# Kernel tuning notes

Hardware: AMD Instinct MI355X
Metric: run time of the kernel (lower is better)

## Reference

```python
import jax, jax.numpy as jnp
import numpy as np

NEG_INF = float(np.finfo(np.float32).min)


def setup_inputs() -> dict:
    key = jax.random.key(0)
    k1, k2, k3 = jax.random.split(key, 3)
    n_context, d_model = 4096, 2048
    x = jax.random.normal(k1, (n_context, d_model), dtype=jnp.float32)
    # nn.Linear default init scale ~ 1/sqrt(fan_in); use small weights for numeric sanity
    W_qk = jax.random.normal(k2, (d_model, d_model), dtype=jnp.float32) / np.sqrt(d_model)
    W_ov = jax.random.normal(k3, (d_model, d_model), dtype=jnp.float32) / np.sqrt(d_model)
    return {"x": x, "W_qk": W_qk, "W_ov": W_ov}


def reference(x, W_qk, W_ov):
    # Faithful to: softmax(X @ W_qk.T @ X.T + causal_mask) @ X @ W_ov.T
    # (biases of the torch Linears are never used in forward)
    n = x.shape[0]
    q = x @ W_qk.T                      # [n, d]
    scores = q @ x.T                    # [n, n]  (no 1/sqrt(d) scaling, as in source)
    causal = jnp.tril(jnp.ones((n, n), dtype=bool))
    scores = jnp.where(causal, scores, NEG_INF)  # additive -inf mask equivalent
    attn = jax.nn.softmax(scores, axis=-1)       # [n, n]
    out = (attn @ x) @ W_ov.T                    # [n, d]
    return out
```

## Files before the change

### kernel.cpp

```cpp
#include <hip/hip_runtime.h>
#include <hip/hip_bf16.h>
#include <stdint.h>
#include <stddef.h>

typedef _Float16 f16;
typedef __attribute__((ext_vector_type(8))) _Float16 f16x8;
typedef __attribute__((ext_vector_type(4))) float    f32x4;

constexpr int BM = 128, BN = 128, BK = 64;

#define GLOAD_LDS16(gp, lp)                                        \
    __builtin_amdgcn_global_load_lds(                              \
        (const __attribute__((address_space(1))) unsigned int*)(gp),\
        (__attribute__((address_space(3))) unsigned int*)(lp), 16, 0, 0)

#define MFMA_TILE(AV, BV)                                                     \
    do {                                                                      \
        __builtin_amdgcn_s_setprio(1);                                        \
        _Pragma("unroll")                                                     \
        for (int mi_ = 0; mi_ < 4; ++mi_)                                     \
            _Pragma("unroll")                                                 \
            for (int ni_ = 0; ni_ < 4; ++ni_)                                 \
                acc[mi_][ni_] = __builtin_amdgcn_mfma_f32_16x16x32_f16(       \
                    (AV)[mi_], (BV)[ni_], acc[mi_][ni_], 0, 0, 0);            \
        __builtin_amdgcn_s_setprio(0);                                        \
    } while (0)

template <int EPI, bool CAUSAL>
__global__ __launch_bounds__(512, 2) void gemm8_a2(
    const f16* __restrict__ Ah, const f16* __restrict__ Al,
    const f16* __restrict__ B,
    float* __restrict__ Cf, f16* __restrict__ Co, f16* __restrict__ Clo,
    int M, int N, int K)
{
    const int bx = blockIdx.x;
    const int by = blockIdx.y;
    if (CAUSAL && 2 * bx > by) return;

    const int tid   = threadIdx.x;
    const int lane  = tid & 63;
    const int wave  = tid >> 6;
    const int wm    = wave >> 2;
    const int wn    = wave & 3;
    const int lrow  = lane & 15;
    const int lquad = lane >> 4;

    __shared__ f16 lds[2][32768];

    const int row0 = by * 128;
    const int col0 = bx * 256;

    const int srow = tid >> 3;
    const int scol = ((tid & 7) ^ (srow & 7)) * 8;
    const int loff = wave * 512;

    const int g0 = ((lquad)     ^ (lrow & 7)) * 8;
    const int g1 = ((4 + lquad) ^ (lrow & 7)) * 8;

    const int arow = (wm * 64 + lrow) * 64;
    const int brow = (wn * 64 + lrow) * 64 + 16384;

    const f16* gAh = Ah + (size_t)(row0 + srow) * K + scol;
    const f16* gAl = Al + (size_t)(row0 + srow) * K + scol;
    const f16* gB  = B  + (size_t)(col0 + srow) * K + scol;
    const size_t r64 = (size_t)64 * K;

    f32x4 acc[4][4];
    const f32x4 fz = {0.f, 0.f, 0.f, 0.f};
    #pragma unroll
    for (int i = 0; i < 4; ++i)
        #pragma unroll
        for (int j = 0; j < 4; ++j) acc[i][j] = fz;

    const int nt = K / 64;

    #pragma unroll
    for (int u = 0; u < 4; ++u)
        GLOAD_LDS16(gB + u * r64, &lds[0][16384 + u * 4096 + loff]);
    #pragma unroll
    for (int u = 0; u < 2; ++u)
        GLOAD_LDS16(gAh + u * r64, &lds[0][u * 4096 + loff]);
    #pragma unroll
    for (int u = 0; u < 2; ++u)
        GLOAD_LDS16(gAl + u * r64, &lds[0][8192 + u * 4096 + loff]);
    asm volatile("s_waitcnt vmcnt(2)");
    __builtin_amdgcn_s_barrier();

    auto tile_body = [&](int t, bool stage) {
        const int cur = t & 1;
        const size_t kn = (size_t)(t + 1) * 64;
        const f16* bufc = &lds[cur][0];
        f16* bufn = &lds[cur ^ 1][0];

        f16x8 av[4], bv0[4], bv1[4];

        #pragma unroll
        for (int mi = 0; mi < 4; ++mi)
            av[mi] = *(const f16x8*)&bufc[arow + mi * 1024 + g0];
        #pragma unroll
        for (int ni = 0; ni < 4; ++ni)
            bv0[ni] = *(const f16x8*)&bufc[brow + ni * 1024 + g0];
        if (stage) {
            GLOAD_LDS16(gB + kn,       &bufn[16384 + loff]);
            GLOAD_LDS16(gB + r64 + kn, &bufn[16384 + 4096 + loff]);
        }
        __builtin_amdgcn_s_barrier();
        asm volatile("s_waitcnt lgkmcnt(0)");
        MFMA_TILE(av, bv0);
        __builtin_amdgcn_s_barrier();

        #pragma unroll
        for (int mi = 0; mi < 4; ++mi)
            av[mi] = *(const f16x8*)&bufc[arow + mi * 1024 + g1];
        #pragma unroll
        for (int ni = 0; ni < 4; ++ni)
            bv1[ni] = *(const f16x8*)&bufc[brow + ni * 1024 + g1];
        if (stage) {
            GLOAD_LDS16(gB + 2 * r64 + kn, &bufn[16384 +  8192 + loff]);
            GLOAD_LDS16(gB + 3 * r64 + kn, &bufn[16384 + 12288 + loff]);
            asm volatile("s_waitcnt vmcnt(4)");
        } else {
            asm volatile("s_waitcnt vmcnt(0)");
        }
        __builtin_amdgcn_s_barrier();
        asm volatile("s_waitcnt lgkmcnt(0)");
        MFMA_TILE(av, bv1);
        __builtin_amdgcn_s_barrier();

        #pragma unroll
        for (int mi = 0; mi < 4; ++mi)
            av[mi] = *(const f16x8*)&bufc[8192 + arow + mi * 1024 + g0];
        if (stage) {
            GLOAD_LDS16(gAh + kn,       &bufn[loff]);
            GLOAD_LDS16(gAh + r64 + kn, &bufn[4096 + loff]);
        }
        __builtin_amdgcn_s_barrier();
        asm volatile("s_waitcnt lgkmcnt(0)");
        MFMA_TILE(av, bv0);
        __builtin_amdgcn_s_barrier();

        #pragma unroll
        for (int mi = 0; mi < 4; ++mi)
            av[mi] = *(const f16x8*)&bufc[8192 + arow + mi * 1024 + g1];
        if (stage) {
            GLOAD_LDS16(gAl + kn,       &bufn[ 8192 + loff]);
            GLOAD_LDS16(gAl + r64 + kn, &bufn[12288 + loff]);
        }
        asm volatile("s_waitcnt vmcnt(2)");
        __builtin_amdgcn_s_barrier();
        asm volatile("s_waitcnt lgkmcnt(0)");
        MFMA_TILE(av, bv1);
        __builtin_amdgcn_s_barrier();
    };

    for (int t = 0; t < nt - 1; ++t) tile_body(t, true);
    tile_body(nt - 1, false);

    #pragma unroll
    for (int mi = 0; mi < 4; ++mi) {
        #pragma unroll
        for (int ni = 0; ni < 4; ++ni) {
            #pragma unroll
            for (int r = 0; r < 4; ++r) {
                const int row = row0 + wm * 64 + mi * 16 + lquad * 4 + r;
                const int col = col0 + wn * 64 + ni * 16 + lrow;
                const size_t idx = (size_t)row * N + col;
                const float v = acc[mi][ni][r];
                if (EPI == 0) {
                    Cf[idx] = v;
                } else {
                    const f16 h = (f16)v;
                    Co[idx]  = h;
                    Clo[idx] = (f16)(v - (float)h);
                }
            }
        }
    }
}

template <int EPI>
__global__ __launch_bounds__(512, 2) void gemm8_1t(
    const f16* __restrict__ A, const f16* __restrict__ B,
    float* __restrict__ Cf, f16* __restrict__ Co,
    int M, int N, int K)
{
    const int bx = blockIdx.x;
    const int by = blockIdx.y;

    const int tid   = threadIdx.x;
    const int lane  = tid & 63;
    const int wave  = tid >> 6;
    const int wm    = wave >> 2;
    const int wn    = wave & 3;
    const int lrow  = lane & 15;
    const int lquad = lane >> 4;

    __shared__ f16 lds[3][24576];

    const int row0 = by * 128;
    const int col0 = bx * 256;

    const int srow = tid >> 3;
    const int scol = ((tid & 7) ^ (srow & 7)) * 8;
    const int loff = wave * 512;
    const int g0 = ((lquad)     ^ (lrow & 7)) * 8;
    const int g1 = ((4 + lquad) ^ (lrow & 7)) * 8;
    const int arow = (wm * 64 + lrow) * 64;
    const int brow = (wn * 64 + lrow) * 64 + 8192;

    const f16* gA = A + (size_t)(row0 + srow) * K + scol;
    const f16* gB = B + (size_t)(col0 + srow) * K + scol;
    const size_t r64 = (size_t)64 * K;

    f32x4 acc[4][4];
    const f32x4 fz = {0.f, 0.f, 0.f, 0.f};
    #pragma unroll
    for (int i = 0; i < 4; ++i)
        #pragma unroll
        for (int j = 0; j < 4; ++j) acc[i][j] = fz;

    const int nt = K / 64;

    #pragma unroll
    for (int tt = 0; tt < 2; ++tt) {
        const size_t kk = (size_t)tt * 64;
        #pragma unroll
        for (int u = 0; u < 4; ++u)
            GLOAD_LDS16(gB + u * r64 + kk, &lds[tt][8192 + u * 4096 + loff]);
        #pragma unroll
        for (int u = 0; u < 2; ++u)
            GLOAD_LDS16(gA + u * r64 + kk, &lds[tt][u * 4096 + loff]);
    }
    asm volatile("s_waitcnt vmcnt(6)");
    __builtin_amdgcn_s_barrier();

    int cur = 0;
    for (int t = 0; t < nt; ++t) {
        const int nb = (cur >= 1) ? (cur - 1) : (cur + 2);
        const bool stage2 = (t + 2 < nt);
        const size_t kn = (size_t)(t + 2) * 64;
        const f16* bufc = &lds[cur][0];
        f16* bufn = &lds[nb][0];

        f16x8 av[4], bv[4];

        #pragma unroll
        for (int mi = 0; mi < 4; ++mi)
            av[mi] = *(const f16x8*)&bufc[arow + mi * 1024 + g0];
        #pragma unroll
        for (int ni = 0; ni < 4; ++ni)
            bv[ni] = *(const f16x8*)&bufc[brow + ni * 1024 + g0];
        if (stage2) {
            GLOAD_LDS16(gB + kn,           &bufn[8192 + loff]);
            GLOAD_LDS16(gB + r64 + kn,     &bufn[8192 + 4096 + loff]);
            GLOAD_LDS16(gB + 2 * r64 + kn, &bufn[8192 + 8192 + loff]);
        }
        __builtin_amdgcn_s_barrier();
        asm volatile("s_waitcnt lgkmcnt(0)");
        MFMA_TILE(av, bv);
        __builtin_amdgcn_s_barrier();

        #pragma unroll
        for (int mi = 0; mi < 4; ++mi)
            av[mi] = *(const f16x8*)&bufc[arow + mi * 1024 + g1];
        #pragma unroll
        for (int ni = 0; ni < 4; ++ni)
            bv[ni] = *(const f16x8*)&bufc[brow + ni * 1024 + g1];
        if (stage2) {
            GLOAD_LDS16(gB + 3 * r64 + kn, &bufn[8192 + 12288 + loff]);
            GLOAD_LDS16(gA + kn,           &bufn[loff]);
            GLOAD_LDS16(gA + r64 + kn,     &bufn[4096 + loff]);
            asm volatile("s_waitcnt vmcnt(6)");
        } else {
            asm volatile("s_waitcnt vmcnt(0)");
        }
        __builtin_amdgcn_s_barrier();
        asm volatile("s_waitcnt lgkmcnt(0)");
        MFMA_TILE(av, bv);
        __builtin_amdgcn_s_barrier();

        cur = (cur == 2) ? 0 : cur + 1;
    }

    #pragma unroll
    for (int mi = 0; mi < 4; ++mi) {
        #pragma unroll
        for (int ni = 0; ni < 4; ++ni) {
            #pragma unroll
            for (int r = 0; r < 4; ++r) {
                const int row = row0 + wm * 64 + mi * 16 + lquad * 4 + r;
                const int col = col0 + wn * 64 + ni * 16 + lrow;
                const size_t idx = (size_t)row * N + col;
                const float v = acc[mi][ni][r];
                if (EPI == 0) Cf[idx] = v;
                else          Co[idx] = (f16)v;
            }
        }
    }
}

template <int EPI, bool KCAUSAL>
__global__ __launch_bounds__(256) void gemm_plain(
    const f16* __restrict__ A, const f16* __restrict__ B,
    float* __restrict__ Cf, f16* __restrict__ Co,
    int M, int N, int K)
{
    const int bx = blockIdx.x;
    const int by = KCAUSAL ? (gridDim.y - 1 - blockIdx.y) : blockIdx.y;

    const int tid   = threadIdx.x;
    const int lane  = tid & 63;
    const int wave  = tid >> 6;
    const int wm    = wave >> 1;
    const int wn    = wave & 1;
    const int lrow  = lane & 15;
    const int lquad = lane >> 4;

    __shared__ f16 sA[BM * BK];
    __shared__ f16 sB[BN * BK];

    const int row0 = by * BM;
    const int col0 = bx * BN;

    const int srow = tid >> 3;
    const int scol = (((tid & 7) ^ ((tid >> 3) & 7))) * 8;
    const int lbase = wave * 512;

    f32x4 acc[4][4];
    const f32x4 fzero = {0.f, 0.f, 0.f, 0.f};
    #pragma unroll
    for (int i = 0; i < 4; ++i)
        #pragma unroll
        for (int j = 0; j < 4; ++j) acc[i][j] = fzero;

    const int Keff = KCAUSAL ? (by + 1) * BM : K;

    for (int k0 = 0; k0 < Keff; k0 += BK) {
        __syncthreads();
        #pragma unroll
        for (int r = 0; r < 4; ++r) {
            const int trow = srow + 32 * r;
            GLOAD_LDS16(&A[(size_t)(row0 + trow) * K + k0 + scol], &sA[lbase + r * 2048]);
            GLOAD_LDS16(&B[(size_t)(col0 + trow) * K + k0 + scol], &sB[lbase + r * 2048]);
        }
        __syncthreads();

        #pragma unroll
        for (int kk = 0; kk < 2; ++kk) {
            const int grpA = ((kk * 4 + lquad) ^ (lrow & 7)) * 8;
            f16x8 av[4], bv[4];
            #pragma unroll
            for (int mi = 0; mi < 4; ++mi)
                av[mi] = *reinterpret_cast<const f16x8*>(
                    &sA[(wm * 64 + mi * 16 + lrow) * BK + grpA]);
            #pragma unroll
            for (int ni = 0; ni < 4; ++ni)
                bv[ni] = *reinterpret_cast<const f16x8*>(
                    &sB[(wn * 64 + ni * 16 + lrow) * BK + grpA]);

            #pragma unroll
            for (int mi = 0; mi < 4; ++mi)
                #pragma unroll
                for (int ni = 0; ni < 4; ++ni)
                    acc[mi][ni] = __builtin_amdgcn_mfma_f32_16x16x32_f16(
                        av[mi], bv[ni], acc[mi][ni], 0, 0, 0);
        }
    }

    #pragma unroll
    for (int mi = 0; mi < 4; ++mi) {
        #pragma unroll
        for (int ni = 0; ni < 4; ++ni) {
            #pragma unroll
            for (int r = 0; r < 4; ++r) {
                const int row = row0 + wm * 64 + mi * 16 + lquad * 4 + r;
                const int col = col0 + wn * 64 + ni * 16 + lrow;
                const size_t idx = (size_t)row * N + col;
                const float v = acc[mi][ni][r];
                if (EPI == 0) Cf[idx] = v;
                else          Co[idx] = (f16)v;
            }
        }
    }
}

__global__ __launch_bounds__(256) void split_f32_f16(
    const float* __restrict__ in, f16* __restrict__ hi, f16* __restrict__ lo,
    size_t nelem)
{
    const size_t i = ((size_t)blockIdx.x * 256 + threadIdx.x) * 4;
    if (i >= nelem) return;
    const float4 v = *reinterpret_cast<const float4*>(in + i);
    union { f16 h[4]; ushort4 u; } H, L;
    H.h[0] = (f16)v.x; H.h[1] = (f16)v.y; H.h[2] = (f16)v.z; H.h[3] = (f16)v.w;
    *reinterpret_cast<ushort4*>(hi + i) = H.u;
    if (lo) {
        L.h[0] = (f16)(v.x - (float)H.h[0]);
        L.h[1] = (f16)(v.y - (float)H.h[1]);
        L.h[2] = (f16)(v.z - (float)H.h[2]);
        L.h[3] = (f16)(v.w - (float)H.h[3]);
        *reinterpret_cast<ushort4*>(lo + i) = L.u;
    }
}

__global__ __launch_bounds__(256) void softmax_rows(
    const float* __restrict__ S, f16* __restrict__ P, int n)
{
    const int row = blockIdx.x;
    const int len = row + 1;
    const int padlen = ((row >> 7) + 1) << 7;
    const float* srow = S + (size_t)row * n;
    f16* prow = P + (size_t)row * n;
    const int tid = threadIdx.x;
    const int lane = tid & 63, wave = tid >> 6;
    __shared__ float redm[4], reds[4];

    float m = -3.0e38f, s = 0.f;
    for (int j = tid; j < len; j += 256) {
        const float v = srow[j];
        const float mn = fmaxf(m, v);
        s = s * __expf(m - mn) + __expf(v - mn);
        m = mn;
    }
    #pragma unroll
    for (int off = 32; off; off >>= 1) {
        const float mo = __shfl_xor(m, off, 64);
        const float so = __shfl_xor(s, off, 64);
        const float mn = fmaxf(m, mo);
        s = s * __expf(m - mn) + so * __expf(mo - mn);
        m = mn;
    }
    if (lane == 0) { redm[wave] = m; reds[wave] = s; }
    __syncthreads();
    float M = redm[0], Sm = reds[0];
    #pragma unroll
    for (int w = 1; w < 4; ++w) {
        const float mn = fmaxf(M, redm[w]);
        Sm = Sm * __expf(M - mn) + reds[w] * __expf(redm[w] - mn);
        M = mn;
    }
    const float inv = 1.0f / Sm;

    const f16 z = (f16)0.0f;
    for (int j = tid; j < padlen; j += 256)
        prow[j] = (j < len) ? (f16)(__expf(srow[j] - M) * inv) : z;
}

__global__ __launch_bounds__(256) void transpose_f32_f16(
    const float* __restrict__ in, f16* __restrict__ out, int rows, int cols)
{
    __shared__ float tile[32][33];
    const int bx = blockIdx.x;
    const int by = blockIdx.y;
    const int tx = threadIdx.x & 31;
    const int ty = threadIdx.x >> 5;
    #pragma unroll
    for (int r = 0; r < 4; ++r)
        tile[ty + 8 * r][tx] = in[(size_t)(by * 32 + ty + 8 * r) * cols + bx * 32 + tx];
    __syncthreads();
    #pragma unroll
    for (int r = 0; r < 4; ++r)
        out[(size_t)(bx * 32 + ty + 8 * r) * rows + by * 32 + tx] =
            (f16)tile[tx][ty + 8 * r];
}

extern "C" void kernel_launch(void* const* d_in, const int* in_sizes, int n_in,
                              void* d_out, int out_size, void* d_ws, size_t ws_size,
                              hipStream_t stream)
{
    const int n = 4096, d = 2048;
    const float* x   = (const float*)d_in[0];
    const float* Wqk = (const float*)d_in[1];
    const float* Wov = (const float*)d_in[2];
    float* out = (float*)d_out;

    char* ws = (char*)d_ws;
    const size_t MB = 1 << 20;
    f16*   xh   = (f16*)  (ws);
    f16*   xl   = (f16*)  (ws + 16 * MB);
    f16*   Wh   = (f16*)  (ws + 32 * MB);
    f16*   Wovh = (f16*)  (ws + 40 * MB);
    f16*   xTh  = (f16*)  (ws + 48 * MB);
    f16*   qh   = (f16*)  (ws + 64 * MB);
    f16*   ql   = (f16*)  (ws + 80 * MB);
    float* S    = (float*)(ws + 96 * MB);
    f16*   P    = (f16*)  (ws);
    f16*   o    = (f16*)  (ws + 64 * MB);

    const dim3 blk(256);
    const dim3 blk8(512);

    split_f32_f16<<<dim3((n * d) / (256 * 4)), blk, 0, stream>>>(x,   xh, xl, (size_t)n * d);
    split_f32_f16<<<dim3((d * d) / (256 * 4)), blk, 0, stream>>>(Wqk, Wh, nullptr, (size_t)d * d);
    split_f32_f16<<<dim3((d * d) / (256 * 4)), blk, 0, stream>>>(Wov, Wovh, nullptr, (size_t)d * d);
    transpose_f32_f16<<<dim3(d / 32, n / 32), blk, 0, stream>>>(x, xTh, n, d);

    gemm8_a2<1, false><<<dim3(d / 256, n / 128), blk8, 0, stream>>>(
        xh, xl, Wh, nullptr, qh, ql, n, d, d);

    gemm8_a2<0, true><<<dim3(n / 256, n / 128), blk8, 0, stream>>>(
        qh, ql, xh, S, nullptr, nullptr, n, n, d);

    softmax_rows<<<dim3(n), blk, 0, stream>>>(S, P, n);

    gemm_plain<2, true><<<dim3(d / BN, n / BM), blk, 0, stream>>>(
        P, xTh, nullptr, o, n, d, n);

    gemm8_1t<0><<<dim3(d / 256, n / 128), blk8, 0, stream>>>(
        o, Wovh, out, nullptr, n, d, d);
}
```

Baseline: 420.1 us.

## Add BK=32 scores GEMM with higher occupancy and per-wave causal skip; cache softmax row

Adds a new gemm32_a2 kernel for the causal scores GEMM. It uses a K-step of 32 and half the LDS, and raises launch_bounds to 4 blocks per CU. Waves whose column slice lies entirely above the diagonal skip the LDS reads, MFMAs and stores. The softmax kernel now caches the row in LDS so global memory is read once instead of twice. The trade-offs are twice as many barrier-synchronised iterations, a full vmcnt(0) wait each step, and 16KB of extra LDS in the softmax kernel, which may lower its occupancy.

```diff
diff --git a/kernel.cpp b/kernel.cpp
--- a/kernel.cpp
+++ b/kernel.cpp
@@ -27,7 +27,7 @@
     } while (0)
 
 template <int EPI, bool CAUSAL>
-__global__ __launch_bounds__(512, 2) void gemm8_a2(
+__global__ __launch_bounds__(512, 4) void gemm32_a2(
     const f16* __restrict__ Ah, const f16* __restrict__ Al,
     const f16* __restrict__ B,
     float* __restrict__ Cf, f16* __restrict__ Co, f16* __restrict__ Clo,
@@ -45,25 +45,27 @@
     const int lrow  = lane & 15;
     const int lquad = lane >> 4;
 
-    __shared__ f16 lds[2][32768];
+    __shared__ f16 lds[2][16384];
 
     const int row0 = by * 128;
     const int col0 = bx * 256;
 
-    const int srow = tid >> 3;
-    const int scol = ((tid & 7) ^ (srow & 7)) * 8;
-    const int loff = wave * 512;
-
-    const int g0 = ((lquad)     ^ (lrow & 7)) * 8;
-    const int g1 = ((4 + lquad) ^ (lrow & 7)) * 8;
-
-    const int arow = (wm * 64 + lrow) * 64;
-    const int brow = (wn * 64 + lrow) * 64 + 16384;
-
-    const f16* gAh = Ah + (size_t)(row0 + srow) * K + scol;
-    const f16* gAl = Al + (size_t)(row0 + srow) * K + scol;
-    const f16* gB  = B  + (size_t)(col0 + srow) * K + scol;
-    const size_t r64 = (size_t)64 * K;
+    const bool liveN = !CAUSAL || (col0 + wn * 64 <= row0 + 127);
+
+    const int srA  = tid >> 3;
+    const int gl   = (tid & 7) ^ (srA & 7);
+    const int term = gl >> 2;
+    const int cg   = gl & 3;
+    const f16* pA = (term ? Al : Ah) + (size_t)(row0 + srA) * K + cg * 8;
+    const f16* pB = B + (size_t)(col0 + 2 * srA + term) * K + cg * 8;
+    const size_t uA = (size_t)64 * K;
+    const size_t uB = (size_t)128 * K;
+    const int ld0 = wave * 512;
+
+    const int aoff0 = (wm * 64 + lrow) * 64 + ((lquad ^ (lrow & 7)) * 8);
+    const int aoff1 = (wm * 64 + lrow) * 64 + (((4 + lquad) ^ (lrow & 7)) * 8);
+    const int boff  = 8192 + (wn * 32 + (lrow >> 1)) * 64 +
+                      ((((lrow & 1) * 4 + lquad) ^ ((lrow >> 1) & 7)) * 8);
 
     f32x4 acc[4][4];
     const f32x4 fz = {0.f, 0.f, 0.f, 0.f};
@@ -72,89 +74,55 @@
         #pragma unroll
         for (int j = 0; j < 4; ++j) acc[i][j] = fz;
 
-    const int nt = K / 64;
-
-    #pragma unroll
-    for (int u = 0; u < 4; ++u)
-        GLOAD_LDS16(gB + u * r64, &lds[0][16384 + u * 4096 + loff]);
-    #pragma unroll
-    for (int u = 0; u < 2; ++u)
-        GLOAD_LDS16(gAh + u * r64, &lds[0][u * 4096 + loff]);
-    #pragma unroll
-    for (int u = 0; u < 2; ++u)
-        GLOAD_LDS16(gAl + u * r64, &lds[0][8192 + u * 4096 + loff]);
-    asm volatile("s_waitcnt vmcnt(2)");
+    const int nt = K / 32;
+
+    GLOAD_LDS16(pA,      &lds[0][ld0]);
+    GLOAD_LDS16(pA + uA, &lds[0][4096 + ld0]);
+    GLOAD_LDS16(pB,      &lds[0][8192 + ld0]);
+    GLOAD_LDS16(pB + uB, &lds[0][12288 + ld0]);
+    asm volatile("s_waitcnt vmcnt(0)");
     __builtin_amdgcn_s_barrier();
 
-    auto tile_body = [&](int t, bool stage) {
-        const int cur = t & 1;
-        const size_t kn = (size_t)(t + 1) * 64;
-        const f16* bufc = &lds[cur][0];
-        f16* bufn = &lds[cur ^ 1][0];
-
-        f16x8 av[4], bv0[4], bv1[4];
-
-        #pragma unroll
-        for (int mi = 0; mi < 4; ++mi)
-            av[mi] = *(const f16x8*)&bufc[arow + mi * 1024 + g0];
-        #pragma unroll
-        for (int ni = 0; ni < 4; ++ni)
-            bv0[ni] = *(const f16x8*)&bufc[brow + ni * 1024 + g0];
+    for (int t = 0; t < nt; ++t) {
+        const f16* bufc = &lds[t & 1][0];
+        f16* bufn = &lds[(t + 1) & 1][0];
+        const bool stage = (t + 1 < nt);
+        const size_t kn = (size_t)(t + 1) * 32;
+
+        f16x8 ah[4], al[4], bv[4];
+
+        if (liveN) {
+            #pragma unroll
+            for (int mi = 0; mi < 4; ++mi)
+                ah[mi] = *(const f16x8*)&bufc[aoff0 + mi * 1024];
+            #pragma unroll
+            for (int ni = 0; ni < 4; ++ni)
+                bv[ni] = *(const f16x8*)&bufc[boff + ni * 512];
+        }
         if (stage) {
-            GLOAD_LDS16(gB + kn,       &bufn[16384 + loff]);
-            GLOAD_LDS16(gB + r64 + kn, &bufn[16384 + 4096 + loff]);
-        }
-        __builtin_amdgcn_s_barrier();
-        asm volatile("s_waitcnt lgkmcnt(0)");
-        MFMA_TILE(av, bv0);
-        __builtin_amdgcn_s_barrier();
-
-        #pragma unroll
-        for (int mi = 0; mi < 4; ++mi)
-            av[mi] = *(const f16x8*)&bufc[arow + mi * 1024 + g1];
-        #pragma unroll
-        for (int ni = 0; ni < 4; ++ni)
-            bv1[ni] = *(const f16x8*)&bufc[brow + ni * 1024 + g1];
-        if (stage) {
-            GLOAD_LDS16(gB + 2 * r64 + kn, &bufn[16384 +  8192 + loff]);
-            GLOAD_LDS16(gB + 3 * r64 + kn, &bufn[16384 + 12288 + loff]);
-            asm volatile("s_waitcnt vmcnt(4)");
-        } else {
-            asm volatile("s_waitcnt vmcnt(0)");
-        }
-        __builtin_amdgcn_s_barrier();
-        asm volatile("s_waitcnt lgkmcnt(0)");
-        MFMA_TILE(av, bv1);
-        __builtin_amdgcn_s_barrier();
-
-        #pragma unroll
-        for (int mi = 0; mi < 4; ++mi)
-            av[mi] = *(const f16x8*)&bufc[8192 + arow + mi * 1024 + g0];
-        if (stage) {
-            GLOAD_LDS16(gAh + kn,       &bufn[loff]);
-            GLOAD_LDS16(gAh + r64 + kn, &bufn[4096 + loff]);
-        }
-        __builtin_amdgcn_s_barrier();
-        asm volatile("s_waitcnt lgkmcnt(0)");
-        MFMA_TILE(av, bv0);
-        __builtin_amdgcn_s_barrier();
-
-        #pragma unroll
-        for (int mi = 0; mi < 4; ++mi)
-            av[mi] = *(const f16x8*)&bufc[8192 + arow + mi * 1024 + g1];
-        if (stage) {
-            GLOAD_LDS16(gAl + kn,       &bufn[ 8192 + loff]);
-            GLOAD_LDS16(gAl + r64 + kn, &bufn[12288 + loff]);
-        }
-        asm volatile("s_waitcnt vmcnt(2)");
-        __builtin_amdgcn_s_barrier();
-        asm volatile("s_waitcnt lgkmcnt(0)");
-        MFMA_TILE(av, bv1);
-        __builtin_amdgcn_s_barrier();
-    };
-
-    for (int t = 0; t < nt - 1; ++t) tile_body(t, true);
-    tile_body(nt - 1, false);
+            GLOAD_LDS16(pA + kn,      &bufn[ld0]);
+            GLOAD_LDS16(pA + uA + kn, &bufn[4096 + ld0]);
+            GLOAD_LDS16(pB + kn,      &bufn[8192 + ld0]);
+            GLOAD_LDS16(pB + uB + kn, &bufn[12288 + ld0]);
+        }
+        __builtin_amdgcn_s_barrier();
+        asm volatile("s_waitcnt lgkmcnt(0)");
+        if (liveN) MFMA_TILE(ah, bv);
+        __builtin_amdgcn_s_barrier();
+
+        if (liveN) {
+            #pragma unroll
+            for (int mi = 0; mi < 4; ++mi)
+                al[mi] = *(const f16x8*)&bufc[aoff1 + mi * 1024];
+        }
+        __builtin_amdgcn_s_barrier();
+        asm volatile("s_waitcnt lgkmcnt(0)");
+        if (liveN) MFMA_TILE(al, bv);
+        if (stage) asm volatile("s_waitcnt vmcnt(0)");
+        __builtin_amdgcn_s_barrier();
+    }
+
+    if (!liveN) return;
 
     #pragma unroll
     for (int mi = 0; mi < 4; ++mi) {
@@ -178,6 +146,158 @@
     }
 }
 
+template <int EPI, bool CAUSAL>
+__global__ __launch_bounds__(512, 2) void gemm8_a2(
+    const f16* __restrict__ Ah, const f16* __restrict__ Al,
+    const f16* __restrict__ B,
+    float* __restrict__ Cf, f16* __restrict__ Co, f16* __restrict__ Clo,
+    int M, int N, int K)
+{
+    const int bx = blockIdx.x;
+    const int by = blockIdx.y;
+    if (CAUSAL && 2 * bx > by) return;
+
+    const int tid   = threadIdx.x;
+    const int lane  = tid & 63;
+    const int wave  = tid >> 6;
+    const int wm    = wave >> 2;
+    const int wn    = wave & 3;
+    const int lrow  = lane & 15;
+    const int lquad = lane >> 4;
+
+    __shared__ f16 lds[2][32768];
+
+    const int row0 = by * 128;
+    const int col0 = bx * 256;
+
+    const int srow = tid >> 3;
+    const int scol = ((tid & 7) ^ (srow & 7)) * 8;
+    const int loff = wave * 512;
+
+    const int g0 = ((lquad)     ^ (lrow & 7)) * 8;
+    const int g1 = ((4 + lquad) ^ (lrow & 7)) * 8;
+
+    const int arow = (wm * 64 + lrow) * 64;
+    const int brow = (wn * 64 + lrow) * 64 + 16384;
+
+    const f16* gAh = Ah + (size_t)(row0 + srow) * K + scol;
+    const f16* gAl = Al + (size_t)(row0 + srow) * K + scol;
+    const f16* gB  = B  + (size_t)(col0 + srow) * K + scol;
+    const size_t r64 = (size_t)64 * K;
+
+    f32x4 acc[4][4];
+    const f32x4 fz = {0.f, 0.f, 0.f, 0.f};
+    #pragma unroll
+    for (int i = 0; i < 4; ++i)
+        #pragma unroll
+        for (int j = 0; j < 4; ++j) acc[i][j] = fz;
+
+    const int nt = K / 64;
+
+    #pragma unroll
+    for (int u = 0; u < 4; ++u)
+        GLOAD_LDS16(gB + u * r64, &lds[0][16384 + u * 4096 + loff]);
+    #pragma unroll
+    for (int u = 0; u < 2; ++u)
+        GLOAD_LDS16(gAh + u * r64, &lds[0][u * 4096 + loff]);
+    #pragma unroll
+    for (int u = 0; u < 2; ++u)
+        GLOAD_LDS16(gAl + u * r64, &lds[0][8192 + u * 4096 + loff]);
+    asm volatile("s_waitcnt vmcnt(2)");
+    __builtin_amdgcn_s_barrier();
+
+    auto tile_body = [&](int t, bool stage) {
+        const int cur = t & 1;
+        const size_t kn = (size_t)(t + 1) * 64;
+        const f16* bufc = &lds[cur][0];
+        f16* bufn = &lds[cur ^ 1][0];
+
+        f16x8 av[4], bv0[4], bv1[4];
+
+        #pragma unroll
+        for (int mi = 0; mi < 4; ++mi)
+            av[mi] = *(const f16x8*)&bufc[arow + mi * 1024 + g0];
+        #pragma unroll
+        for (int ni = 0; ni < 4; ++ni)
+            bv0[ni] = *(const f16x8*)&bufc[brow + ni * 1024 + g0];
+        if (stage) {
+            GLOAD_LDS16(gB + kn,       &bufn[16384 + loff]);
+            GLOAD_LDS16(gB + r64 + kn, &bufn[16384 + 4096 + loff]);
+        }
+        __builtin_amdgcn_s_barrier();
+        asm volatile("s_waitcnt lgkmcnt(0)");
+        MFMA_TILE(av, bv0);
+        __builtin_amdgcn_s_barrier();
+
+        #pragma unroll
+        for (int mi = 0; mi < 4; ++mi)
+            av[mi] = *(const f16x8*)&bufc[arow + mi * 1024 + g1];
+        #pragma unroll
+        for (int ni = 0; ni < 4; ++ni)
+            bv1[ni] = *(const f16x8*)&bufc[brow + ni * 1024 + g1];
+        if (stage) {
+            GLOAD_LDS16(gB + 2 * r64 + kn, &bufn[16384 +  8192 + loff]);
+            GLOAD_LDS16(gB + 3 * r64 + kn, &bufn[16384 + 12288 + loff]);
+            asm volatile("s_waitcnt vmcnt(4)");
+        } else {
+            asm volatile("s_waitcnt vmcnt(0)");
+        }
+        __builtin_amdgcn_s_barrier();
+        asm volatile("s_waitcnt lgkmcnt(0)");
+        MFMA_TILE(av, bv1);
+        __builtin_amdgcn_s_barrier();
+
+        #pragma unroll
+        for (int mi = 0; mi < 4; ++mi)
+            av[mi] = *(const f16x8*)&bufc[8192 + arow + mi * 1024 + g0];
+        if (stage) {
+            GLOAD_LDS16(gAh + kn,       &bufn[loff]);
+            GLOAD_LDS16(gAh + r64 + kn, &bufn[4096 + loff]);
+        }
+        __builtin_amdgcn_s_barrier();
+        asm volatile("s_waitcnt lgkmcnt(0)");
+        MFMA_TILE(av, bv0);
+        __builtin_amdgcn_s_barrier();
+
+        #pragma unroll
+        for (int mi = 0; mi < 4; ++mi)
+            av[mi] = *(const f16x8*)&bufc[8192 + arow + mi * 1024 + g1];
+        if (stage) {
+            GLOAD_LDS16(gAl + kn,       &bufn[ 8192 + loff]);
+            GLOAD_LDS16(gAl + r64 + kn, &bufn[12288 + loff]);
+        }
+        asm volatile("s_waitcnt vmcnt(2)");
+        __builtin_amdgcn_s_barrier();
+        asm volatile("s_waitcnt lgkmcnt(0)");
+        MFMA_TILE(av, bv1);
+        __builtin_amdgcn_s_barrier();
+    };
+
+    for (int t = 0; t < nt - 1; ++t) tile_body(t, true);
+    tile_body(nt - 1, false);
+
+    #pragma unroll
+    for (int mi = 0; mi < 4; ++mi) {
+        #pragma unroll
+        for (int ni = 0; ni < 4; ++ni) {
+            #pragma unroll
+            for (int r = 0; r < 4; ++r) {
+                const int row = row0 + wm * 64 + mi * 16 + lquad * 4 + r;
+                const int col = col0 + wn * 64 + ni * 16 + lrow;
+                const size_t idx = (size_t)row * N + col;
+                const float v = acc[mi][ni][r];
+                if (EPI == 0) {
+                    Cf[idx] = v;
+                } else {
+                    const f16 h = (f16)v;
+                    Co[idx]  = h;
+                    Clo[idx] = (f16)(v - (float)h);
+                }
+            }
+        }
+    }
+}
+
 template <int EPI>
 __global__ __launch_bounds__(512, 2) void gemm8_1t(
     const f16* __restrict__ A, const f16* __restrict__ B,
@@ -413,11 +533,13 @@
     f16* prow = P + (size_t)row * n;
     const int tid = threadIdx.x;
     const int lane = tid & 63, wave = tid >> 6;
+    __shared__ float rowbuf[4096];
     __shared__ float redm[4], reds[4];
 
     float m = -3.0e38f, s = 0.f;
     for (int j = tid; j < len; j += 256) {
         const float v = srow[j];
+        rowbuf[j] = v;
         const float mn = fmaxf(m, v);
         s = s * __expf(m - mn) + __expf(v - mn);
         m = mn;
@@ -443,7 +565,7 @@
 
     const f16 z = (f16)0.0f;
     for (int j = tid; j < padlen; j += 256)
-        prow[j] = (j < len) ? (f16)(__expf(srow[j] - M) * inv) : z;
+        prow[j] = (j < len) ? (f16)(__expf(rowbuf[j] - M) * inv) : z;
 }
 
 __global__ __launch_bounds__(256) void transpose_f32_f16(
@@ -498,7 +620,7 @@
     gemm8_a2<1, false><<<dim3(d / 256, n / 128), blk8, 0, stream>>>(
         xh, xl, Wh, nullptr, qh, ql, n, d, d);
 
-    gemm8_a2<0, true><<<dim3(n / 256, n / 128), blk8, 0, stream>>>(
+    gemm32_a2<0, true><<<dim3(n / 256, n / 128), blk8, 0, stream>>>(
         qh, ql, xh, S, nullptr, nullptr, n, n, d);
 
     softmax_rows<<<dim3(n), blk, 0, stream>>>(S, P, n);
```

Result: slower. 440.9 us (+5.0%).
